# Performance work log

Measured on AMD Instinct MI355X. Metric: run time of the kernel, lower is better.

The kernel has to match this reference:

```python
import jax, jax.numpy as jnp
import numpy as np

B, T, SD = 16, 512, 64          # batch, action seq len, sample_dim
EMB, HD = 1024, 64              # emb_dim, head_dim
NH = EMB // HD                  # 16 heads
DEPTH, NREG, LAT, FF = 8, 16, 256, 4 * EMB
S = T + NREG                    # total sequence length (actions + registers)


def setup_inputs() -> dict:
    key = jax.random.key(0)
    ks = jax.random.split(key, 16)
    def n(k, shape, scale=0.02):
        return jax.random.normal(k, shape, jnp.float32) * scale
    return {
        "sample": jax.random.normal(ks[0], (B, T, SD), jnp.float32),
        "W_emb": n(ks[1], (SD, EMB)), "b_emb": jnp.zeros((EMB,), jnp.float32),
        "pos": n(ks[2], (T, EMB)),
        "registers": n(ks[3], (NREG, EMB), 1.0),
        "ln1_s": jnp.ones((DEPTH, EMB), jnp.float32), "ln1_b": jnp.zeros((DEPTH, EMB), jnp.float32),
        "W_qkv": n(ks[4], (DEPTH, EMB, 3 * EMB)), "b_qkv": jnp.zeros((DEPTH, 3 * EMB), jnp.float32),
        "W_o": n(ks[5], (DEPTH, EMB, EMB)), "b_o": jnp.zeros((DEPTH, EMB), jnp.float32),
        "ln2_s": jnp.ones((DEPTH, EMB), jnp.float32), "ln2_b": jnp.zeros((DEPTH, EMB), jnp.float32),
        "W_fc1": n(ks[6], (DEPTH, EMB, FF)), "b_fc1": jnp.zeros((DEPTH, FF), jnp.float32),
        "W_fc2": n(ks[7], (DEPTH, FF, EMB)), "b_fc2": jnp.zeros((DEPTH, EMB), jnp.float32),
        "lnf_s": jnp.ones((EMB,), jnp.float32), "lnf_b": jnp.zeros((EMB,), jnp.float32),
        "W_head": n(ks[8], (EMB, LAT)), "b_head": jnp.zeros((LAT,), jnp.float32),
    }


def _ln(x, s, b):
    m = jnp.mean(x, -1, keepdims=True)
    v = jnp.var(x, -1, keepdims=True)
    return (x - m) * jax.lax.rsqrt(v + 1e-5) * s + b


def _causal_last_mask():
    # True = attended to. Actions attend to all actions but NOT registers;
    # registers attend to all actions and causally (incl. self) to registers.
    allowed = jnp.ones((S, S), jnp.bool_)
    allowed = allowed.at[:T, T:].set(False)
    allowed = allowed.at[T:, T:].set(jnp.tril(jnp.ones((NREG, NREG), jnp.bool_)))
    return allowed


def reference(sample, W_emb, b_emb, pos, registers, ln1_s, ln1_b, W_qkv, b_qkv,
              W_o, b_o, ln2_s, ln2_b, W_fc1, b_fc1, W_fc2, b_fc2,
              lnf_s, lnf_b, W_head, b_head):
    # embed + positional add
    x = sample @ W_emb + b_emb + pos[None, :, :]          # [B,T,E]
    # concat registers
    x = jnp.concatenate([x, jnp.broadcast_to(registers, (B, NREG, EMB))], axis=1)  # [B,S,E]
    mask = _causal_last_mask()                             # [S,S]
    scale = 1.0 / jnp.sqrt(jnp.asarray(HD, x.dtype))
    for i in range(DEPTH):
        # pre-LN multi-head attention with structured block mask
        h = _ln(x, ln1_s[i], ln1_b[i])
        qkv = h @ W_qkv[i] + b_qkv[i]
        q, k, v = jnp.split(qkv, 3, axis=-1)
        q = q.reshape(B, S, NH, HD)
        k = k.reshape(B, S, NH, HD)
        v = v.reshape(B, S, NH, HD)
        att = jnp.einsum('bqhd,bkhd->bhqk', q, k) * scale
        att = jnp.where(mask[None, None], att, jnp.finfo(att.dtype).min)
        att = jax.nn.softmax(att, axis=-1)
        o = jnp.einsum('bhqk,bkhd->bqhd', att, v).reshape(B, S, EMB)
        x = x + o @ W_o[i] + b_o[i]
        # pre-LN MLP
        h2 = _ln(x, ln2_s[i], ln2_b[i])
        x = x + jax.nn.gelu(h2 @ W_fc1[i] + b_fc1[i]) @ W_fc2[i] + b_fc2[i]
    x = _ln(x, lnf_s, lnf_b)
    # head applied to register positions only
    return x[:, T:] @ W_head + b_head                      # [B,NREG,LAT]
```

## Files before the change

### kernel.cpp

```cpp
#include <hip/hip_runtime.h>
#include <hip/hip_bf16.h>


typedef unsigned short u16;
typedef __attribute__((ext_vector_type(4))) float f32x4;
typedef __attribute__((ext_vector_type(8))) __bf16 bf16x8;

#define DEV static __device__ __forceinline__

constexpr int Bb = 16, Tt = 512, E = 1024, HD = 64, NHd = 16;
constexpr int DEPTH = 8, NREG = 16, LAT = 256, FF = 4096;
constexpr int S = Tt + NREG;
constexpr int SPAD = 576;
constexpr int MR = Bb * S;
constexpr int ME = Bb * Tt;

DEV u16 f2bf(float f) {
  unsigned u = __builtin_bit_cast(unsigned, f);
  u += 0x7fffu + ((u >> 16) & 1u);
  return (u16)(u >> 16);
}

DEV void gll16(const u16* g, u16* l) {
  __builtin_amdgcn_global_load_lds((const __attribute__((address_space(1))) void*)g,
                                   (__attribute__((address_space(3))) void*)l, 16, 0, 0);
}

enum { M_EMBED, M_QKV, M_OPROJ, M_FC1, M_FC2, M_HEAD };

struct GA {
  const u16* A; const u16* Bt;
  int K, lda, ldb, Nrows, ldc;
  const float* bias; const float* pos;
  float* fout; u16* bout;
  u16 *qp, *kp, *vtp;
};

template<int MODE>
__global__ __launch_bounds__(256)
void gemm_bt(GA g) {
  __shared__ __align__(16) u16 As[128 * 32];
  __shared__ __align__(16) u16 Bs[128 * 32];
  const int tid = threadIdx.x;
  const u16* A  = g.A;
  const u16* Bt = g.Bt;
  const int tM = blockIdx.y, tN = blockIdx.x;
  const int lane = tid & 63, wid = tid >> 6;
  const int wr = wid >> 1, wc = wid & 1;
  const int fr = lane & 15, fg = lane >> 4;

  const int arow = tM * 128 + (tid >> 2);
  int br0 = tN * 128 + (tid >> 2);
  int br1 = br0 + 64;
  if (br0 > g.Nrows - 1) br0 = g.Nrows - 1;
  if (br1 > g.Nrows - 1) br1 = g.Nrows - 1;
  const int kseg = (tid & 3) * 8;
  u16* lA = As + (tid & 192) * 8;
  u16* lB = Bs + (tid & 192) * 8;

  f32x4 acc[4][4];
#pragma unroll
  for (int i = 0; i < 4; ++i)
#pragma unroll
    for (int j = 0; j < 4; ++j) acc[i][j] = f32x4{0.f, 0.f, 0.f, 0.f};

  const int nk = g.K >> 5;
  for (int kt = 0; kt < nk; ++kt) {
    const int k0 = kt << 5;
    gll16(A  + (long)arow        * g.lda + k0 + kseg, lA);
    gll16(A  + (long)(arow + 64) * g.lda + k0 + kseg, lA + 2048);
    gll16(Bt + (long)br0         * g.ldb + k0 + kseg, lB);
    gll16(Bt + (long)br1         * g.ldb + k0 + kseg, lB + 2048);
    __syncthreads();
    bf16x8 af[4], bfr[4];
#pragma unroll
    for (int mi = 0; mi < 4; ++mi)
      af[mi] = *(const bf16x8*)&As[(wr * 64 + mi * 16 + fr) * 32 + fg * 8];
#pragma unroll
    for (int ni = 0; ni < 4; ++ni)
      bfr[ni] = *(const bf16x8*)&Bs[(wc * 64 + ni * 16 + fr) * 32 + fg * 8];
#pragma unroll
    for (int mi = 0; mi < 4; ++mi)
#pragma unroll
      for (int ni = 0; ni < 4; ++ni)
        acc[mi][ni] = __builtin_amdgcn_mfma_f32_16x16x32_bf16(af[mi], bfr[ni], acc[mi][ni], 0, 0, 0);
    __syncthreads();
  }

#pragma unroll
  for (int mi = 0; mi < 4; ++mi)
#pragma unroll
    for (int ni = 0; ni < 4; ++ni)
#pragma unroll
      for (int j = 0; j < 4; ++j) {
        const int row = tM * 128 + wr * 64 + mi * 16 + fg * 4 + j;
        const int col = tN * 128 + wc * 64 + ni * 16 + fr;
        float v = acc[mi][ni][j];
        if (MODE == M_EMBED) {
          const int b = row >> 9, t = row & 511;
          v += g.bias[col] + g.pos[(long)t * E + col];
          g.fout[((long)(b * S + t)) * E + col] = v;
        } else if (MODE == M_QKV) {
          const int b = row / S, s = row - b * S;
          v += g.bias[col];
          const int part = col >> 10, c = col & 1023;
          const int hh = c >> 6, d = c & 63;
          const u16 bf = f2bf(v);
          if (part == 0)      g.qp [((long)((b * NHd + hh) * SPAD + s)) * HD + d] = bf;
          else if (part == 1) g.kp [((long)((b * NHd + hh) * SPAD + s)) * HD + d] = bf;
          else                g.vtp[((long)((b * NHd + hh) * HD   + d)) * SPAD + s] = bf;
        } else if (MODE == M_OPROJ || MODE == M_FC2) {
          const long idx = (long)row * g.ldc + col;
          g.fout[idx] += v + g.bias[col];
        } else if (MODE == M_FC1) {
          v += g.bias[col];
          const float z = 0.7978845608028654f * (v + 0.044715f * v * v * v);
          const float e = __expf(2.f * z);
          const float th = 1.f - 2.f / (e + 1.f);
          g.bout[(long)row * g.ldc + col] = f2bf(0.5f * v * (1.f + th));
        } else if (MODE == M_HEAD) {
          g.fout[(long)row * g.ldc + col] = v + g.bias[col];
        }
      }
}

__global__ __launch_bounds__(256)
void flash_k(const u16* __restrict__ q, const u16* __restrict__ k,
             const u16* __restrict__ vt, u16* __restrict__ o) {
  __shared__ __align__(16) u16 Ks[64 * 64];
  __shared__ __align__(16) u16 Vs[64 * 64];
  __shared__ __align__(16) u16 Ps[4 * 16 * 64];
  const int tid = threadIdx.x;
  const int lane = tid & 63, w = tid >> 6;
  const int fr = lane & 15, fg = lane >> 4;
  const int qt = blockIdx.x, bh = blockIdx.y;
  const int q0 = qt * 64;

  const u16* qrow = q + ((long)bh * SPAD + q0 + w * 16 + fr) * HD;
  const bf16x8 qf0 = *(const bf16x8*)(qrow + fg * 8);
  const bf16x8 qf1 = *(const bf16x8*)(qrow + 32 + fg * 8);

  const int srow = lane >> 3, sseg = (lane & 7) * 8;
  const u16* kg = k  + ((long)bh * SPAD + w * 16 + srow) * HD + sseg;
  const u16* vg = vt + ((long)(bh * HD + w * 16 + srow)) * SPAD + sseg;
  u16* lk = Ks + w * 16 * HD;
  u16* lv = Vs + w * 16 * HD;

  float m[4], lsum[4]; f32x4 oa[4];
#pragma unroll
  for (int j = 0; j < 4; ++j) { m[j] = -1e30f; lsum[j] = 0.f; }
#pragma unroll
  for (int n = 0; n < 4; ++n) oa[n] = f32x4{0.f, 0.f, 0.f, 0.f};

  const int nt = (q0 < Tt) ? 8 : 9;
  for (int kt = 0; kt < nt; ++kt) {
    __syncthreads();
    gll16(kg + kt * 64 * HD,          lk);
    gll16(kg + kt * 64 * HD + 8 * HD, lk + 8 * HD);
    gll16(vg + kt * 64,               lv);
    gll16(vg + kt * 64 + 8 * SPAD,    lv + 8 * HD);
    __syncthreads();

    f32x4 sfr[4];
#pragma unroll
    for (int n = 0; n < 4; ++n) {
      const bf16x8 kf0 = *(const bf16x8*)&Ks[(n * 16 + fr) * HD + fg * 8];
      const bf16x8 kf1 = *(const bf16x8*)&Ks[(n * 16 + fr) * HD + 32 + fg * 8];
      sfr[n] = __builtin_amdgcn_mfma_f32_16x16x32_bf16(qf0, kf0, f32x4{0.f,0.f,0.f,0.f}, 0, 0, 0);
      sfr[n] = __builtin_amdgcn_mfma_f32_16x16x32_bf16(qf1, kf1, sfr[n], 0, 0, 0);
    }
    float p[4][4];
#pragma unroll
    for (int j = 0; j < 4; ++j) {
      const int qg = q0 + w * 16 + fg * 4 + j;
      const int vlim = qg < Tt ? Tt : qg + 1;
#pragma unroll
      for (int n = 0; n < 4; ++n) {
        const int col = kt * 64 + n * 16 + fr;
        p[n][j] = (col < vlim) ? sfr[n][j] * 0.125f : -1e30f;
      }
    }
#pragma unroll
    for (int j = 0; j < 4; ++j) {
      float pm = fmaxf(fmaxf(p[0][j], p[1][j]), fmaxf(p[2][j], p[3][j]));
#pragma unroll
      for (int msk = 1; msk <= 8; msk <<= 1) pm = fmaxf(pm, __shfl_xor(pm, msk));
      const float mn = fmaxf(m[j], pm);
      const float corr = __expf(m[j] - mn);
      m[j] = mn;
      float rs = 0.f;
#pragma unroll
      for (int n = 0; n < 4; ++n) { const float e = __expf(p[n][j] - mn); p[n][j] = e; rs += e; }
#pragma unroll
      for (int msk = 1; msk <= 8; msk <<= 1) rs += __shfl_xor(rs, msk);
      lsum[j] = lsum[j] * corr + rs;
#pragma unroll
      for (int n = 0; n < 4; ++n) oa[n][j] *= corr;
    }
#pragma unroll
    for (int j = 0; j < 4; ++j)
#pragma unroll
      for (int n = 0; n < 4; ++n)
        Ps[w * 1024 + (fg * 4 + j) * 64 + n * 16 + fr] = f2bf(p[n][j]);
    __syncthreads();
    const bf16x8 pf0 = *(const bf16x8*)&Ps[w * 1024 + fr * 64 + fg * 8];
    const bf16x8 pf1 = *(const bf16x8*)&Ps[w * 1024 + fr * 64 + 32 + fg * 8];
#pragma unroll
    for (int n = 0; n < 4; ++n) {
      const bf16x8 vf0 = *(const bf16x8*)&Vs[(n * 16 + fr) * HD + fg * 8];
      const bf16x8 vf1 = *(const bf16x8*)&Vs[(n * 16 + fr) * HD + 32 + fg * 8];
      oa[n] = __builtin_amdgcn_mfma_f32_16x16x32_bf16(pf0, vf0, oa[n], 0, 0, 0);
      oa[n] = __builtin_amdgcn_mfma_f32_16x16x32_bf16(pf1, vf1, oa[n], 0, 0, 0);
    }
  }

  const int b = bh >> 4, hh = bh & 15;
#pragma unroll
  for (int j = 0; j < 4; ++j) {
    const int qg = q0 + w * 16 + fg * 4 + j;
    if (qg < S) {
      const float inv = 1.f / lsum[j];
#pragma unroll
      for (int n = 0; n < 4; ++n)
        o[((long)(b * S + qg)) * E + hh * HD + n * 16 + fr] = f2bf(oa[n][j] * inv);
    }
  }
}

__global__ __launch_bounds__(256)
void ln_k(const float* __restrict__ x, const float* __restrict__ sc,
          const float* __restrict__ bi, u16* __restrict__ out, int gather) {
  const int r = blockIdx.x;
  const int srow = gather ? ((r >> 4) * S + Tt + (r & 15)) : r;
  const float4 v = ((const float4*)(x + (long)srow * E))[threadIdx.x];
  float s = v.x + v.y + v.z + v.w;
  float q = v.x * v.x + v.y * v.y + v.z * v.z + v.w * v.w;
#pragma unroll
  for (int o = 32; o; o >>= 1) { s += __shfl_down(s, o); q += __shfl_down(q, o); }
  __shared__ float ps[8];
  if ((threadIdx.x & 63) == 0) { ps[threadIdx.x >> 6] = s; ps[4 + (threadIdx.x >> 6)] = q; }
  __syncthreads();
  s = ps[0] + ps[1] + ps[2] + ps[3];
  q = ps[4] + ps[5] + ps[6] + ps[7];
  const float mean = s * (1.f / E);
  const float rs = rsqrtf(q * (1.f / E) - mean * mean + 1e-5f);
  const int c = threadIdx.x * 4;
  ushort4 o4;
  o4.x = f2bf((v.x - mean) * rs * sc[c + 0] + bi[c + 0]);
  o4.y = f2bf((v.y - mean) * rs * sc[c + 1] + bi[c + 1]);
  o4.z = f2bf((v.z - mean) * rs * sc[c + 2] + bi[c + 2]);
  o4.w = f2bf((v.w - mean) * rs * sc[c + 3] + bi[c + 3]);
  ((ushort4*)(out + (long)r * E))[threadIdx.x] = o4;
}

__global__ __launch_bounds__(256)
void wtrans(const float* __restrict__ src, u16* __restrict__ dst, int R, int C) {
  __shared__ float t[32][33];
  const int c0 = blockIdx.x * 32, r0 = blockIdx.y * 32;
  const int tx = threadIdx.x & 31, ty = threadIdx.x >> 5;
#pragma unroll
  for (int i = 0; i < 32; i += 8) t[ty + i][tx] = src[(long)(r0 + ty + i) * C + c0 + tx];
  __syncthreads();
#pragma unroll
  for (int i = 0; i < 32; i += 8) dst[(long)(c0 + ty + i) * R + r0 + tx] = f2bf(t[tx][ty + i]);
}

__global__ void cvt_bf(const float* __restrict__ in, u16* __restrict__ out, long n) {
  const long i = ((long)blockIdx.x * blockDim.x + threadIdx.x) * 4;
  if (i >= n) return;
  const float4 v = *(const float4*)(in + i);
  ushort4 o; o.x = f2bf(v.x); o.y = f2bf(v.y); o.z = f2bf(v.z); o.w = f2bf(v.w);
  *(ushort4*)(out + i) = o;
}

__global__ void zero_k(float4* p, long n) {
  long i = (long)blockIdx.x * blockDim.x + threadIdx.x;
  const long st = (long)gridDim.x * blockDim.x;
  const float4 z = make_float4(0.f, 0.f, 0.f, 0.f);
  for (; i < n; i += st) p[i] = z;
}

__global__ void reg_copy(const float* __restrict__ regs, float* __restrict__ x) {
  const int b = blockIdx.x >> 4, r = blockIdx.x & 15;
  const float4* sp = (const float4*)(regs + (long)r * E);
  float4* dp = (float4*)(x + ((long)(b * S + Tt + r)) * E);
  dp[threadIdx.x] = sp[threadIdx.x];
}

constexpr long OFF_WQKV = 0L;
constexpr long OFF_WO   = OFF_WQKV + 3072L * 1024 * 2;
constexpr long OFF_WFC1 = OFF_WO   + 1024L * 1024 * 2;
constexpr long OFF_WFC2 = OFF_WFC1 + 4096L * 1024 * 2;
constexpr long OFF_WEMB = OFF_WFC2 + 1024L * 4096 * 2;
constexpr long OFF_WHEAD= OFF_WEMB + 1024L * 64 * 2;
constexpr long OFF_SMP  = OFF_WHEAD+ 256L * 1024 * 2;
constexpr long OFF_X    = OFF_SMP  + (long)ME * 64 * 2;
constexpr long OFF_H    = OFF_X    + (long)MR * E * 4;
constexpr long OFF_Q    = OFF_H    + (long)MR * E * 2;
constexpr long OFF_K    = OFF_Q    + 256L * SPAD * HD * 2;
constexpr long OFF_VT   = OFF_K    + 256L * SPAD * HD * 2;
constexpr long OFF_O    = OFF_VT   + 256L * SPAD * HD * 2;
constexpr long OFF_HF   = OFF_O    + (long)MR * FF * 2;
constexpr long WS_NEED  = OFF_HF   + 256L * 1024 * 2;

extern "C" void kernel_launch(void* const* d_in, const int* in_sizes, int n_in,
                              void* d_out, int out_size, void* d_ws, size_t ws_size,
                              hipStream_t stream) {
  if (ws_size < (size_t)WS_NEED) return;

  const float* sample = (const float*)d_in[0];
  const float* W_emb  = (const float*)d_in[1];
  const float* b_emb  = (const float*)d_in[2];
  const float* pos    = (const float*)d_in[3];
  const float* regs   = (const float*)d_in[4];
  const float* ln1_s  = (const float*)d_in[5];
  const float* ln1_b  = (const float*)d_in[6];
  const float* W_qkv  = (const float*)d_in[7];
  const float* b_qkv  = (const float*)d_in[8];
  const float* W_o    = (const float*)d_in[9];
  const float* b_o    = (const float*)d_in[10];
  const float* ln2_s  = (const float*)d_in[11];
  const float* ln2_b  = (const float*)d_in[12];
  const float* W_fc1  = (const float*)d_in[13];
  const float* b_fc1  = (const float*)d_in[14];
  const float* W_fc2  = (const float*)d_in[15];
  const float* b_fc2  = (const float*)d_in[16];
  const float* lnf_s  = (const float*)d_in[17];
  const float* lnf_b  = (const float*)d_in[18];
  const float* W_head = (const float*)d_in[19];
  const float* b_head = (const float*)d_in[20];

  char* w = (char*)d_ws;
  u16* wqkvT = (u16*)(w + OFF_WQKV);
  u16* woT   = (u16*)(w + OFF_WO);
  u16* wfc1T = (u16*)(w + OFF_WFC1);
  u16* wfc2T = (u16*)(w + OFF_WFC2);
  u16* wembT = (u16*)(w + OFF_WEMB);
  u16* wheadT= (u16*)(w + OFF_WHEAD);
  u16* smp   = (u16*)(w + OFF_SMP);
  float* x   = (float*)(w + OFF_X);
  u16* h     = (u16*)(w + OFF_H);
  u16* qp    = (u16*)(w + OFF_Q);
  u16* kp    = (u16*)(w + OFF_K);
  u16* vtp   = (u16*)(w + OFF_VT);
  u16* o     = (u16*)(w + OFF_O);
  u16* a1    = (u16*)(w + OFF_O);
  u16* hf    = (u16*)(w + OFF_HF);

  wtrans<<<dim3(32, 2, 1), 256, 0, stream>>>(W_emb,  wembT, 64, 1024);
  wtrans<<<dim3(8, 32, 1), 256, 0, stream>>>(W_head, wheadT, 1024, 256);
  cvt_bf<<<dim3(512), 256, 0, stream>>>(sample, smp, (long)ME * 64);
  zero_k<<<dim3(2048), 256, 0, stream>>>((float4*)qp, (3L * 256 * SPAD * HD * 2) / 16);

  {
    GA g{}; g.A = smp; g.Bt = wembT; g.K = 64; g.lda = 64; g.ldb = 64;
    g.Nrows = E; g.bias = b_emb; g.pos = pos; g.fout = x;
    gemm_bt<M_EMBED><<<dim3(8, 64, 1), 256, 0, stream>>>(g);
  }
  reg_copy<<<dim3(256), 256, 0, stream>>>(regs, x);

  for (int L = 0; L < DEPTH; ++L) {
    wtrans<<<dim3(96, 32, 1),  256, 0, stream>>>(W_qkv + (long)L * 1024 * 3072, wqkvT, 1024, 3072);
    wtrans<<<dim3(32, 32, 1),  256, 0, stream>>>(W_o   + (long)L * 1024 * 1024, woT,   1024, 1024);
    wtrans<<<dim3(128, 32, 1), 256, 0, stream>>>(W_fc1 + (long)L * 1024 * 4096, wfc1T, 1024, 4096);
    wtrans<<<dim3(32, 128, 1), 256, 0, stream>>>(W_fc2 + (long)L * 4096 * 1024, wfc2T, 4096, 1024);

    ln_k<<<dim3(MR), 256, 0, stream>>>(x, ln1_s + L * E, ln1_b + L * E, h, 0);
    {
      GA g{}; g.A = h; g.Bt = wqkvT;
      g.K = 1024; g.lda = 1024; g.ldb = 1024; g.Nrows = 3072;
      g.bias = b_qkv + L * 3072; g.qp = qp; g.kp = kp; g.vtp = vtp;
      gemm_bt<M_QKV><<<dim3(24, 66, 1), 256, 0, stream>>>(g);
    }
    flash_k<<<dim3(9, 256, 1), 256, 0, stream>>>(qp, kp, vtp, o);
    {
      GA g{}; g.A = o; g.Bt = woT;
      g.K = 1024; g.lda = 1024; g.ldb = 1024; g.Nrows = 1024; g.ldc = 1024;
      g.bias = b_o + L * E; g.fout = x;
      gemm_bt<M_OPROJ><<<dim3(8, 66, 1), 256, 0, stream>>>(g);
    }
    ln_k<<<dim3(MR), 256, 0, stream>>>(x, ln2_s + L * E, ln2_b + L * E, h, 0);
    {
      GA g{}; g.A = h; g.Bt = wfc1T;
      g.K = 1024; g.lda = 1024; g.ldb = 1024; g.Nrows = 4096; g.ldc = 4096;
      g.bias = b_fc1 + L * FF; g.bout = a1;
      gemm_bt<M_FC1><<<dim3(32, 66, 1), 256, 0, stream>>>(g);
    }
    {
      GA g{}; g.A = a1; g.Bt = wfc2T;
      g.K = 4096; g.lda = 4096; g.ldb = 4096; g.Nrows = 1024; g.ldc = 1024;
      g.bias = b_fc2 + L * E; g.fout = x;
      gemm_bt<M_FC2><<<dim3(8, 66, 1), 256, 0, stream>>>(g);
    }
  }

  ln_k<<<dim3(256), 256, 0, stream>>>(x, lnf_s, lnf_b, hf, 1);
  {
    GA g{}; g.A = hf; g.Bt = wheadT; g.K = 1024; g.lda = 1024; g.ldb = 1024;
    g.Nrows = LAT; g.ldc = LAT; g.bias = b_head; g.fout = (float*)d_out;
    gemm_bt<M_HEAD><<<dim3(2, 2, 1), 256, 0, stream>>>(g);
  }
}
```

Baseline: 4.422 ms.

## Split-K residual GEMMs with atomic accumulation and XCD-aware tile remapping

Splits the K dimension of the output-projection GEMM (2 ways) and the FC2 GEMM (4 ways) across the grid's z dimension. Partial results are accumulated into the fp32 residual stream with atomicAdd, and only the first split adds the bias. It also remaps the flat workgroup index so that consecutive tiles land on the same XCD, aiming for better L2 reuse. This adds parallelism to the narrow N=1024 GEMMs at the cost of atomic traffic and a non-deterministic float summation order.

```diff
diff --git a/kernel.cpp b/kernel.cpp
--- a/kernel.cpp
+++ b/kernel.cpp
@@ -30,7 +30,7 @@
 
 struct GA {
   const u16* A; const u16* Bt;
-  int K, lda, ldb, Nrows, ldc;
+  int K, Kc, lda, ldb, Nrows, ldc;
   const float* bias; const float* pos;
   float* fout; u16* bout;
   u16 *qp, *kp, *vtp;
@@ -42,9 +42,19 @@
   __shared__ __align__(16) u16 As[128 * 32];
   __shared__ __align__(16) u16 Bs[128 * 32];
   const int tid = threadIdx.x;
-  const u16* A  = g.A;
-  const u16* Bt = g.Bt;
-  const int tM = blockIdx.y, tN = blockIdx.x;
+  const int kz = blockIdx.z;
+  const u16* A  = g.A  + (long)kz * g.Kc;
+  const u16* Bt = g.Bt + (long)kz * g.Kc;
+
+  const int nwg = gridDim.x * gridDim.y;
+  int flat = blockIdx.y * gridDim.x + blockIdx.x;
+  {
+    const int q = nwg >> 3, r = nwg & 7;
+    const int xcd = flat & 7, loc = flat >> 3;
+    flat = (xcd < r ? xcd * (q + 1) : r * (q + 1) + (xcd - r) * q) + loc;
+  }
+  const int tM = flat / gridDim.x, tN = flat % gridDim.x;
+
   const int lane = tid & 63, wid = tid >> 6;
   const int wr = wid >> 1, wc = wid & 1;
   const int fr = lane & 15, fg = lane >> 4;
@@ -64,7 +74,7 @@
 #pragma unroll
     for (int j = 0; j < 4; ++j) acc[i][j] = f32x4{0.f, 0.f, 0.f, 0.f};
 
-  const int nk = g.K >> 5;
+  const int nk = g.Kc >> 5;
   for (int kt = 0; kt < nk; ++kt) {
     const int k0 = kt << 5;
     gll16(A  + (long)arow        * g.lda + k0 + kseg, lA);
@@ -110,8 +120,8 @@
           else if (part == 1) g.kp [((long)((b * NHd + hh) * SPAD + s)) * HD + d] = bf;
           else                g.vtp[((long)((b * NHd + hh) * HD   + d)) * SPAD + s] = bf;
         } else if (MODE == M_OPROJ || MODE == M_FC2) {
-          const long idx = (long)row * g.ldc + col;
-          g.fout[idx] += v + g.bias[col];
+          if (kz == 0) v += g.bias[col];
+          atomicAdd(&g.fout[(long)row * g.ldc + col], v);
         } else if (MODE == M_FC1) {
           v += g.bias[col];
           const float z = 0.7978845608028654f * (v + 0.044715f * v * v * v);
@@ -353,7 +363,7 @@
   zero_k<<<dim3(2048), 256, 0, stream>>>((float4*)qp, (3L * 256 * SPAD * HD * 2) / 16);
 
   {
-    GA g{}; g.A = smp; g.Bt = wembT; g.K = 64; g.lda = 64; g.ldb = 64;
+    GA g{}; g.A = smp; g.Bt = wembT; g.K = 64; g.Kc = 64; g.lda = 64; g.ldb = 64;
     g.Nrows = E; g.bias = b_emb; g.pos = pos; g.fout = x;
     gemm_bt<M_EMBED><<<dim3(8, 64, 1), 256, 0, stream>>>(g);
   }
@@ -368,35 +378,35 @@
     ln_k<<<dim3(MR), 256, 0, stream>>>(x, ln1_s + L * E, ln1_b + L * E, h, 0);
     {
       GA g{}; g.A = h; g.Bt = wqkvT;
-      g.K = 1024; g.lda = 1024; g.ldb = 1024; g.Nrows = 3072;
+      g.K = 1024; g.Kc = 1024; g.lda = 1024; g.ldb = 1024; g.Nrows = 3072;
       g.bias = b_qkv + L * 3072; g.qp = qp; g.kp = kp; g.vtp = vtp;
       gemm_bt<M_QKV><<<dim3(24, 66, 1), 256, 0, stream>>>(g);
     }
     flash_k<<<dim3(9, 256, 1), 256, 0, stream>>>(qp, kp, vtp, o);
     {
       GA g{}; g.A = o; g.Bt = woT;
-      g.K = 1024; g.lda = 1024; g.ldb = 1024; g.Nrows = 1024; g.ldc = 1024;
+      g.K = 1024; g.Kc = 512; g.lda = 1024; g.ldb = 1024; g.Nrows = 1024; g.ldc = 1024;
       g.bias = b_o + L * E; g.fout = x;
-      gemm_bt<M_OPROJ><<<dim3(8, 66, 1), 256, 0, stream>>>(g);
+      gemm_bt<M_OPROJ><<<dim3(8, 66, 2), 256, 0, stream>>>(g);
     }
     ln_k<<<dim3(MR), 256, 0, stream>>>(x, ln2_s + L * E, ln2_b + L * E, h, 0);
     {
       GA g{}; g.A = h; g.Bt = wfc1T;
-      g.K = 1024; g.lda = 1024; g.ldb = 1024; g.Nrows = 4096; g.ldc = 4096;
+      g.K = 1024; g.Kc = 1024; g.lda = 1024; g.ldb = 1024; g.Nrows = 4096; g.ldc = 4096;
       g.bias = b_fc1 + L * FF; g.bout = a1;
       gemm_bt<M_FC1><<<dim3(32, 66, 1), 256, 0, stream>>>(g);
     }
     {
       GA g{}; g.A = a1; g.Bt = wfc2T;
-      g.K = 4096; g.lda = 4096; g.ldb = 4096; g.Nrows = 1024; g.ldc = 1024;
+      g.K = 4096; g.Kc = 1024; g.lda = 4096; g.ldb = 4096; g.Nrows = 1024; g.ldc = 1024;
       g.bias = b_fc2 + L * E; g.fout = x;
-      gemm_bt<M_FC2><<<dim3(8, 66, 1), 256, 0, stream>>>(g);
+      gemm_bt<M_FC2><<<dim3(8, 66, 4), 256, 0, stream>>>(g);
     }
   }
 
   ln_k<<<dim3(256), 256, 0, stream>>>(x, lnf_s, lnf_b, hf, 1);
   {
-    GA g{}; g.A = hf; g.Bt = wheadT; g.K = 1024; g.lda = 1024; g.ldb = 1024;
+    GA g{}; g.A = hf; g.Bt = wheadT; g.K = 1024; g.Kc = 1024; g.lda = 1024; g.ldb = 1024;
     g.Nrows = LAT; g.ldc = LAT; g.bias = b_head; g.fout = (float*)d_out;
     gemm_bt<M_HEAD><<<dim3(2, 2, 1), 256, 0, stream>>>(g);
   }
```

Result: slower. 4.816 ms (+8.9%).
